# Performance work log

Measured on AMD Instinct MI355X. Metric: run time of the kernel, lower is better.

The kernel has to match this reference:

```python
import jax, jax.numpy as jnp
import numpy as np

DECAY = 0.99
EPS = 1e-5
K = 512  # num_embeddings


def setup_inputs() -> dict:
    key = jax.random.key(0)
    k1, k2, k3 = jax.random.split(key, 3)
    B, C, H, W = 32, 64, 64, 64
    x = jax.random.normal(k1, (B, C, H, W), dtype=jnp.float32)
    codebook = jax.random.uniform(k2, (K, C), dtype=jnp.float32)
    ema_cluster_size = jnp.ones((K,), dtype=jnp.float32)
    ema_weight = jax.random.uniform(k3, (K, C), dtype=jnp.float32)
    return {"x": x, "codebook": codebook,
            "ema_cluster_size": ema_cluster_size, "ema_weight": ema_weight}


def reference(x, codebook, ema_cluster_size, ema_weight):
    B, C, H, W = x.shape
    # (B, C, H, W) -> (B*H*W, C)
    x_flat = jnp.transpose(x, (0, 2, 3, 1)).reshape(-1, C)

    x_sq = jnp.sum(x_flat * x_flat, axis=1, keepdims=True)        # [N, 1]
    e_sq = jnp.sum(codebook * codebook, axis=1)[None, :]          # [1, K]
    distances = x_sq + e_sq - 2.0 * (x_flat @ codebook.T)         # [N, K]
    indices = jnp.argmin(distances, axis=1)                        # [N]

    quantized = codebook[indices].reshape(B, H, W, C)
    quantized = jnp.transpose(quantized, (0, 3, 1, 2))             # [B, C, H, W]

    # EMA codebook update (training path); one-hot matmuls expressed as segment sums
    counts = jax.ops.segment_sum(jnp.ones_like(indices, dtype=x.dtype), indices,
                                 num_segments=K)                   # [K]
    sums = jax.ops.segment_sum(x_flat, indices, num_segments=K)    # [K, C]
    new_cluster_size = DECAY * ema_cluster_size + (1.0 - DECAY) * counts
    new_ema_weight = DECAY * ema_weight + (1.0 - DECAY) * sums
    n = jnp.sum(new_cluster_size)
    smoothed = (new_cluster_size + EPS) / (n + K * EPS) * n
    new_codebook = new_ema_weight / smoothed[:, None]

    commitment_loss = jnp.mean((x - jax.lax.stop_gradient(quantized)) ** 2)
    unique_codes = jnp.sum(counts > 0).astype(jnp.float32)

    out = x + jax.lax.stop_gradient(quantized - x)  # straight-through estimator
    return out, commitment_loss, unique_codes, new_codebook
```

## Files before the change

kernel.cpp:

```cpp
#include <hip/hip_runtime.h>


typedef __attribute__((ext_vector_type(8))) short bf16x8;
typedef __attribute__((ext_vector_type(16))) float f32x16;

#define MFMA32 __builtin_amdgcn_mfma_f32_32x32x16_bf16

__device__ __forceinline__ unsigned short f2bf(float f) {
    unsigned u = __float_as_uint(f);
    return (unsigned short)((u + 0x7fffu + ((u >> 16) & 1u)) >> 16);
}
__device__ __forceinline__ float bf2f(unsigned short h) {
    return __uint_as_float(((unsigned)h) << 16);
}

__device__ __forceinline__ void upd(float s, int kq, float& b1, int& q1, float& b2, int& q2) {
    bool t1 = s < b1;
    bool t2 = s < b2;
    float nb2 = t1 ? b1 : (t2 ? s : b2);
    int   nq2 = t1 ? q1 : (t2 ? kq : q2);
    b2 = nb2; q2 = nq2;
    b1 = t1 ? s : b1;
    q1 = t1 ? kq : q1;
}

__device__ __forceinline__ int refine_pair(int k1, int k2, long gx,
        const float* __restrict__ x, const float* __restrict__ cbg,
        const float* esq) {
    const float4* e1 = (const float4*)(cbg + (k1 << 6));
    const float4* e2 = (const float4*)(cbg + (k2 << 6));
    float a0 = 0.f, a1 = 0.f, c0 = 0.f, c1 = 0.f;
    #pragma unroll 4
    for (int j = 0; j < 16; ++j) {
        float4 ea = e1[j], eb = e2[j];
        float x0 = x[gx + (long)(4 * j + 0) * 4096];
        float x1 = x[gx + (long)(4 * j + 1) * 4096];
        float x2 = x[gx + (long)(4 * j + 2) * 4096];
        float x3 = x[gx + (long)(4 * j + 3) * 4096];
        a0 = fmaf(x0, ea.x, a0); a1 = fmaf(x1, ea.y, a1);
        a0 = fmaf(x2, ea.z, a0); a1 = fmaf(x3, ea.w, a1);
        c0 = fmaf(x0, eb.x, c0); c1 = fmaf(x1, eb.y, c1);
        c0 = fmaf(x2, eb.z, c0); c1 = fmaf(x3, eb.w, c1);
    }
    float s1 = esq[k1] - 2.f * (a0 + a1);
    float s2 = esq[k2] - 2.f * (c0 + c1);
    return (s2 < s1 || (s2 == s1 && k2 < k1)) ? k2 : k1;
}

#define AM_LDS_FLOATS 33280

__global__ void __launch_bounds__(512, 1)
vq_argmin(const float* __restrict__ x, const float* __restrict__ cbg,
          unsigned short* __restrict__ bkg, float* __restrict__ zero528) {
    extern __shared__ float lds[];
    float* esq = lds + 32768;
    bf16x8* chi = (bf16x8*)lds;
    bf16x8* clo = (bf16x8*)(lds + 16384);
    const int tid  = threadIdx.x;
    const int lane = tid & 63;
    const int wv   = tid >> 6;
    const int l31  = lane & 31;
    const int hh   = lane >> 5;

    {
        const float4* rowp = (const float4*)(cbg + (tid << 6));
        float s = 0.f;
        #pragma unroll
        for (int u = 0; u < 8; ++u) {
            float4 va = rowp[u * 2], vb = rowp[u * 2 + 1];
            const float v[8] = {va.x, va.y, va.z, va.w, vb.x, vb.y, vb.z, vb.w};
            bf16x8 h8, l8;
            #pragma unroll
            for (int j = 0; j < 8; ++j) {
                float e = v[j];
                s = fmaf(e, e, s);
                unsigned short hb = f2bf(e);
                float lo = e - bf2f(hb);
                h8[j] = (short)hb;
                l8[j] = (short)f2bf(lo);
            }
            chi[u * 512 + tid] = h8;
            clo[u * 512 + tid] = l8;
        }
        esq[tid] = s;
    }
    zero528[tid] = 0.f;
    if (tid < 16) zero528[512 + tid] = 0.f;

    const int nb = blockIdx.x * 512 + wv * 64;
    bf16x8 B0h[4], B0l[4], B1h[4], B1l[4];
    #pragma unroll
    for (int ct = 0; ct < 2; ++ct) {
        const int n = nb + ct * 32 + l31;
        const long gx = (long)(n >> 12) * 262144 + (long)((n >> 6) & 63) * 64 + (n & 63);
        #pragma unroll
        for (int cs = 0; cs < 4; ++cs) {
            float v[8];
            #pragma unroll
            for (int j = 0; j < 8; ++j)
                v[j] = -2.f * x[gx + (long)(cs * 16 + hh * 8 + j) * 4096];
            union { unsigned u[4]; bf16x8 v8; } uh, ul;
            #pragma unroll
            for (int p = 0; p < 4; ++p) {
                unsigned hp, lp;
                asm("v_cvt_pk_bf16_f32 %0, %1, %2" : "=v"(hp) : "v"(v[2*p]), "v"(v[2*p+1]));
                float r0 = v[2*p]     - __uint_as_float(hp << 16);
                float r1 = v[2*p + 1] - __uint_as_float(hp & 0xFFFF0000u);
                asm("v_cvt_pk_bf16_f32 %0, %1, %2" : "=v"(lp) : "v"(r0), "v"(r1));
                uh.u[p] = hp; ul.u[p] = lp;
            }
            if (ct == 0) { B0h[cs] = uh.v8; B0l[cs] = ul.v8; }
            else         { B1h[cs] = uh.v8; B1l[cs] = ul.v8; }
        }
    }
    __syncthreads();

    float b1a = 3.4e38f, b2a = 3.4e38f, b1b = 3.4e38f, b2b = 3.4e38f;
    int   q1a = 0, q2a = 0, q1b = 0, q2b = 0;
    bf16x8 Xh[4], Xl[4], Yh[4], Yl[4];

#define LOADA(Ah, Al, kt) { _Pragma("unroll") for (int cs = 0; cs < 4; ++cs) { \
        const int fi = (cs * 2 + hh) * 512 + (kt) * 32 + l31; \
        Ah[cs] = chi[fi]; Al[cs] = clo[fi]; } }

#define STEP(Ah, Al, kt) { \
        f32x16 acc0, acc1; \
        _Pragma("unroll") for (int g = 0; g < 4; ++g) { \
            float4 e4 = *(const float4*)(esq + (kt) * 32 + 8 * g + 4 * hh); \
            acc0[4*g] = e4.x; acc0[4*g+1] = e4.y; acc0[4*g+2] = e4.z; acc0[4*g+3] = e4.w; \
            acc1[4*g] = e4.x; acc1[4*g+1] = e4.y; acc1[4*g+2] = e4.z; acc1[4*g+3] = e4.w; } \
        _Pragma("unroll") for (int cs = 0; cs < 4; ++cs) { \
            acc0 = MFMA32(Ah[cs], B0h[cs], acc0, 0, 0, 0); \
            acc1 = MFMA32(Ah[cs], B1h[cs], acc1, 0, 0, 0); \
            acc0 = MFMA32(Al[cs], B0h[cs], acc0, 0, 0, 0); \
            acc1 = MFMA32(Al[cs], B1h[cs], acc1, 0, 0, 0); \
            acc0 = MFMA32(Ah[cs], B0l[cs], acc0, 0, 0, 0); \
            acc1 = MFMA32(Ah[cs], B1l[cs], acc1, 0, 0, 0); } \
        _Pragma("unroll") for (int e = 0; e < 16; ++e) { \
            int kq = (kt) * 32 + (e & 3) + 8 * (e >> 2); \
            upd(acc0[e], kq, b1a, q1a, b2a, q2a); \
            upd(acc1[e], kq, b1b, q1b, b2b, q2b); } }

    LOADA(Xh, Xl, 0)
    #pragma unroll 1
    for (int ktp = 0; ktp < 16; ktp += 2) {
        LOADA(Yh, Yl, ktp + 1)
        STEP(Xh, Xl, ktp)
        if (ktp + 2 < 16) LOADA(Xh, Xl, ktp + 2)
        STEP(Yh, Yl, ktp + 1)
    }

#define MERGE(b1, q1, b2, q2, ct) { \
        float mb1 = b1, mb2 = b2; int mk1 = q1 + 4 * hh, mk2 = q2 + 4 * hh; \
        float ob1 = __shfl_xor(mb1, 32, 64); int ok1 = __shfl_xor(mk1, 32, 64); \
        float ob2 = __shfl_xor(mb2, 32, 64); int ok2 = __shfl_xor(mk2, 32, 64); \
        bool t = (ob1 < mb1) || (ob1 == mb1 && ok1 < mk1); \
        float w1 = t ? ob1 : mb1;  int wk1 = t ? ok1 : mk1; \
        float l1 = t ? mb1 : ob1;  int lk1 = t ? mk1 : ok1; \
        float w2c = t ? ob2 : mb2; int wk2c = t ? ok2 : mk2; \
        bool t2 = (w2c < l1) || (w2c == l1 && wk2c < lk1); \
        float w2 = t2 ? w2c : l1;  int wk2 = t2 ? wk2c : lk1; \
        if (hh == 0) { \
            int kk = wk1; \
            if (wk2 != wk1 && (w2 - w1 < 2e-3f)) { \
                const int n = nb + (ct) * 32 + l31; \
                const long gx = (long)(n >> 12) * 262144 \
                              + (long)((n >> 6) & 63) * 64 + (n & 63); \
                kk = refine_pair(wk1, wk2, gx, x, cbg, esq); \
            } \
            bkg[nb + (ct) * 32 + l31] = (unsigned short)kk; } }

    MERGE(b1a, q1a, b2a, q2a, 0)
    MERGE(b1b, q1b, b2b, q2b, 1)
#undef LOADA
#undef STEP
#undef MERGE
}

#define FUSED_LDS_BYTES (33536 * 2)

__global__ void __launch_bounds__(512)
vq_fused(const float* __restrict__ x, const float* __restrict__ cbg,
         const unsigned short* __restrict__ bkg, float* __restrict__ out,
         float* __restrict__ hsum, float* __restrict__ acc_loss,
         float* __restrict__ slabs) {
    extern __shared__ unsigned short sm16[];
    const int tid = threadIdx.x;
    if (blockIdx.x < 256) {
        float* hist = (float*)sm16;
        float* lred = (float*)sm16 + 512;
        hist[tid] = 0.f;
        __syncthreads();
        const int n  = blockIdx.x * 512 + tid;
        const long gx = (long)(n >> 12) * 262144 + (long)((n >> 6) & 63) * 64 + (n & 63);
        const int k1 = bkg[n];
        atomicAdd(&hist[k1], 1.0f);
        const float4* q4 = (const float4*)(cbg + (k1 << 6));
        float lsum = 0.f;
        #pragma unroll
        for (int j = 0; j < 16; ++j) {
            float4 q = q4[j];
            const float qv[4] = {q.x, q.y, q.z, q.w};
            #pragma unroll
            for (int r = 0; r < 4; ++r) {
                const int c = 4 * j + r;
                float xc = x[gx + (long)c * 4096];
                out[gx + (long)c * 4096] = qv[r];
                float d = xc - qv[r];
                lsum = fmaf(d, d, lsum);
            }
        }
        #pragma unroll
        for (int o = 32; o > 0; o >>= 1) lsum += __shfl_down(lsum, o, 64);
        if ((tid & 63) == 0) lred[tid >> 6] = lsum;
        __syncthreads();
        if (tid == 0) {
            float l = ((lred[0] + lred[1]) + (lred[2] + lred[3]))
                    + ((lred[4] + lred[5]) + (lred[6] + lred[7]));
            atomicAdd(acc_loss, l);
        }
        { float v = hist[tid]; if (v != 0.f) atomicAdd(&hsum[tid], v); }
    } else {
        unsigned short* xb = sm16;
        unsigned short* kb = sm16 + 33024;
        const int lane = tid & 63;
        const int w    = tid >> 6;
        const int l31  = lane & 31;
        const int hh   = lane >> 5;
        const int bix  = blockIdx.x - 256;
        const int n0   = bix * 512;
        const float* xpl = x + (long)(n0 >> 12) * 262144 + (n0 & 4095);

        kb[tid] = bkg[n0 + tid];
        #pragma unroll
        for (int i = 0; i < 16; ++i) {
            const int f  = tid + i * 512;
            const int c  = f >> 7;
            const int n4 = (f & 127) << 2;
            float4 v = *(const float4*)(xpl + (long)c * 4096 + n4);
            ushort4 o;
            o.x = f2bf(v.x); o.y = f2bf(v.y); o.z = f2bf(v.z); o.w = f2bf(v.w);
            *(ushort4*)(xb + c * 516 + n4) = o;
        }
        __syncthreads();

        const int t0 = w * 32 + l31;
        const int t1 = (w + 8) * 32 + l31;
        f32x16 aA0 = {}, aA1 = {}, aB0 = {}, aB1 = {};

        #pragma unroll 1
        for (int b16 = 0; b16 < 32; ++b16) {
            const int nofs = b16 * 16 + hh * 8;
            ushort4 p0a = *(const ushort4*)(xb + l31 * 516 + nofs);
            ushort4 p0b = *(const ushort4*)(xb + l31 * 516 + nofs + 4);
            ushort4 p1a = *(const ushort4*)(xb + (32 + l31) * 516 + nofs);
            ushort4 p1b = *(const ushort4*)(xb + (32 + l31) * 516 + nofs + 4);
            bf16x8 Bf0, Bf1;
            Bf0[0] = (short)p0a.x; Bf0[1] = (short)p0a.y;
            Bf0[2] = (short)p0a.z; Bf0[3] = (short)p0a.w;
            Bf0[4] = (short)p0b.x; Bf0[5] = (short)p0b.y;
            Bf0[6] = (short)p0b.z; Bf0[7] = (short)p0b.w;
            Bf1[0] = (short)p1a.x; Bf1[1] = (short)p1a.y;
            Bf1[2] = (short)p1a.z; Bf1[3] = (short)p1a.w;
            Bf1[4] = (short)p1b.x; Bf1[5] = (short)p1b.y;
            Bf1[6] = (short)p1b.z; Bf1[7] = (short)p1b.w;
            ushort4 k4a = *(const ushort4*)(kb + nofs);
            ushort4 k4b = *(const ushort4*)(kb + nofs + 4);
            const int kk[8] = {k4a.x, k4a.y, k4a.z, k4a.w,
                               k4b.x, k4b.y, k4b.z, k4b.w};
            bf16x8 A0, A1;
            #pragma unroll
            for (int j = 0; j < 8; ++j) {
                A0[j] = (kk[j] == t0) ? (short)0x3F80 : (short)0;
                A1[j] = (kk[j] == t1) ? (short)0x3F80 : (short)0;
            }
            aA0 = MFMA32(A0, Bf0, aA0, 0, 0, 0);
            aA1 = MFMA32(A0, Bf1, aA1, 0, 0, 0);
            aB0 = MFMA32(A1, Bf0, aB0, 0, 0, 0);
            aB1 = MFMA32(A1, Bf1, aB1, 0, 0, 0);
        }
        float* slab = slabs + (long)bix * 32768;
        #pragma unroll
        for (int e = 0; e < 16; ++e) {
            const int row = (e & 3) + 8 * (e >> 2) + 4 * hh;
            slab[(w * 32 + row) * 64 + l31]            = aA0[e];
            slab[(w * 32 + row) * 64 + 32 + l31]       = aA1[e];
            slab[((w + 8) * 32 + row) * 64 + l31]      = aB0[e];
            slab[((w + 8) * 32 + row) * 64 + 32 + l31] = aB1[e];
        }
    }
}

__global__ void __launch_bounds__(512)
vq_final(const float* __restrict__ slabs, const float* __restrict__ hsum,
         const float* __restrict__ acc_loss, const float* __restrict__ ema_cs,
         const float* __restrict__ ema_w, float* __restrict__ out_scalars,
         float* __restrict__ out_cb) {
    __shared__ float sm[512];
    __shared__ float s_red[17];
    const int tid = threadIdx.x;
    float cnt = hsum[tid];
    float ncs = 0.99f * ema_cs[tid] + 0.01f * cnt;
    float v1 = ncs;
    float v2 = (cnt > 0.f) ? 1.f : 0.f;
    #pragma unroll
    for (int o = 32; o > 0; o >>= 1) {
        v1 += __shfl_down(v1, o, 64);
        v2 += __shfl_down(v2, o, 64);
    }
    const int wv = tid >> 6;
    if ((tid & 63) == 0) { s_red[wv] = v1; s_red[wv + 8] = v2; }
    __syncthreads();
    if (tid == 0) {
        float nn = 0.f, uq = 0.f;
        #pragma unroll
        for (int i = 0; i < 8; ++i) { nn += s_red[i]; uq += s_red[i + 8]; }
        s_red[16] = nn;
        if (blockIdx.x == 0) {
            out_scalars[0] = acc_loss[0] / 8388608.f;
            out_scalars[1] = uq;
        }
    }
    __syncthreads();
    float nn = s_red[16];
    sm[tid] = (ncs + 1e-5f) / (nn + 512.f * 1e-5f) * nn;
    __syncthreads();
    const int e = blockIdx.x * 512 + tid;
    float s = 0.f;
    #pragma unroll 8
    for (int b = 0; b < 256; ++b) s += slabs[(long)b * 32768 + e];
    float nw = 0.99f * ema_w[e] + 0.01f * s;
    out_cb[e] = nw / sm[e >> 6];
}

extern "C" void kernel_launch(void* const* d_in, const int* in_sizes, int n_in,
                              void* d_out, int out_size, void* d_ws, size_t ws_size,
                              hipStream_t stream) {
    const float* x      = (const float*)d_in[0];
    const float* cb     = (const float*)d_in[1];
    const float* ema_cs = (const float*)d_in[2];
    const float* ema_w  = (const float*)d_in[3];

    float* out     = (float*)d_out;
    float* scalars = out + 8388608;
    float* out_cb  = out + 8388610;
    float* ws      = (float*)d_ws;

    float* slabs    = ws;
    float* hsum     = slabs + 8388608;
    float* acc_loss = hsum + 512;
    unsigned short* bkg = (unsigned short*)(acc_loss + 16);

    vq_argmin<<<256, 512, AM_LDS_FLOATS * sizeof(float), stream>>>(x, cb, bkg, hsum);
    vq_fused<<<512, 512, FUSED_LDS_BYTES, stream>>>(x, cb, bkg, out, hsum, acc_loss, slabs);
    vq_final<<<64, 512, 0, stream>>>(slabs, hsum, acc_loss, ema_cs, ema_w, scalars, out_cb);
}
```

Measured before the change: 89.33 us.

## Precompute split-bf16 codebook in prep kernel and halve argmin block work for occupancy

```diff
diff --git a/kernel.cpp b/kernel.cpp
--- a/kernel.cpp
+++ b/kernel.cpp
@@ -12,6 +12,39 @@
 }
 __device__ __forceinline__ float bf2f(unsigned short h) {
     return __uint_as_float(((unsigned)h) << 16);
+}
+
+__global__ void __launch_bounds__(512)
+vq_prep(const float* __restrict__ cb, float* __restrict__ esq, char* __restrict__ cbF) {
+    __shared__ float tile[64 * 65];
+    const int tid = threadIdx.x;
+    const int k0  = blockIdx.x * 64;
+    #pragma unroll
+    for (int i = tid; i < 4096; i += 512)
+        tile[(i >> 6) * 65 + (i & 63)] = cb[k0 * 64 + i];
+    __syncthreads();
+    const int u  = tid >> 6;
+    const int kl = tid & 63;
+    const float* row = tile + kl * 65;
+    const int cbase = (u >> 1) * 16 + (u & 1) * 8;
+    bf16x8 h8, l8;
+    #pragma unroll
+    for (int j = 0; j < 8; ++j) {
+        float e = row[cbase + j];
+        unsigned short hb = f2bf(e);
+        float lo = e - bf2f(hb);
+        h8[j] = (short)hb;
+        l8[j] = (short)f2bf(lo);
+    }
+    const size_t idx = (size_t)(u * 512 + k0 + kl) * 16;
+    *(bf16x8*)(cbF + idx)         = h8;
+    *(bf16x8*)(cbF + 65536 + idx) = l8;
+    if (u == 0) {
+        float s = 0.f;
+        #pragma unroll
+        for (int c = 0; c < 64; ++c) { float v = row[c]; s = fmaf(v, v, s); }
+        esq[k0 + kl] = s;
+    }
 }
 
 __device__ __forceinline__ void upd(float s, int kq, float& b1, int& q1, float& b2, int& q2) {
@@ -47,15 +80,16 @@
     return (s2 < s1 || (s2 == s1 && k2 < k1)) ? k2 : k1;
 }
 
-#define AM_LDS_FLOATS 33280
-
-__global__ void __launch_bounds__(512, 1)
+#define AM_LDS_FLOATS 16896
+
+__global__ void __launch_bounds__(512, 2)
 vq_argmin(const float* __restrict__ x, const float* __restrict__ cbg,
+          const float* __restrict__ esqg, const char* __restrict__ cbF,
           unsigned short* __restrict__ bkg, float* __restrict__ zero528) {
     extern __shared__ float lds[];
-    float* esq = lds + 32768;
-    bf16x8* chi = (bf16x8*)lds;
-    bf16x8* clo = (bf16x8*)(lds + 16384);
+    float* esq = lds + 16384;
+    const bf16x8* chi   = (const bf16x8*)lds;
+    const bf16x8* clo_g = (const bf16x8*)(cbF + 65536);
     const int tid  = threadIdx.x;
     const int lane = tid & 63;
     const int wv   = tid >> 6;
@@ -63,35 +97,19 @@
     const int hh   = lane >> 5;
 
     {
-        const float4* rowp = (const float4*)(cbg + (tid << 6));
-        float s = 0.f;
-        #pragma unroll
-        for (int u = 0; u < 8; ++u) {
-            float4 va = rowp[u * 2], vb = rowp[u * 2 + 1];
-            const float v[8] = {va.x, va.y, va.z, va.w, vb.x, vb.y, vb.z, vb.w};
-            bf16x8 h8, l8;
-            #pragma unroll
-            for (int j = 0; j < 8; ++j) {
-                float e = v[j];
-                s = fmaf(e, e, s);
-                unsigned short hb = f2bf(e);
-                float lo = e - bf2f(hb);
-                h8[j] = (short)hb;
-                l8[j] = (short)f2bf(lo);
-            }
-            chi[u * 512 + tid] = h8;
-            clo[u * 512 + tid] = l8;
-        }
-        esq[tid] = s;
+        const float4* src = (const float4*)cbF;
+        float4* dst = (float4*)lds;
+        #pragma unroll
+        for (int i = tid; i < 4096; i += 512) dst[i] = src[i];
+        esq[tid] = esqg[tid];
     }
     zero528[tid] = 0.f;
     if (tid < 16) zero528[512 + tid] = 0.f;
 
-    const int nb = blockIdx.x * 512 + wv * 64;
-    bf16x8 B0h[4], B0l[4], B1h[4], B1l[4];
-    #pragma unroll
-    for (int ct = 0; ct < 2; ++ct) {
-        const int n = nb + ct * 32 + l31;
+    const int nb = blockIdx.x * 256 + wv * 32;
+    bf16x8 Bh[4], Bl[4];
+    {
+        const int n = nb + l31;
         const long gx = (long)(n >> 12) * 262144 + (long)((n >> 6) & 63) * 64 + (n & 63);
         #pragma unroll
         for (int cs = 0; cs < 4; ++cs) {
@@ -109,72 +127,67 @@
                 asm("v_cvt_pk_bf16_f32 %0, %1, %2" : "=v"(lp) : "v"(r0), "v"(r1));
                 uh.u[p] = hp; ul.u[p] = lp;
             }
-            if (ct == 0) { B0h[cs] = uh.v8; B0l[cs] = ul.v8; }
-            else         { B1h[cs] = uh.v8; B1l[cs] = ul.v8; }
-        }
-    }
-    __syncthreads();
-
-    float b1a = 3.4e38f, b2a = 3.4e38f, b1b = 3.4e38f, b2b = 3.4e38f;
-    int   q1a = 0, q2a = 0, q1b = 0, q2b = 0;
-    bf16x8 Xh[4], Xl[4], Yh[4], Yl[4];
-
-#define LOADA(Ah, Al, kt) { _Pragma("unroll") for (int cs = 0; cs < 4; ++cs) { \
-        const int fi = (cs * 2 + hh) * 512 + (kt) * 32 + l31; \
-        Ah[cs] = chi[fi]; Al[cs] = clo[fi]; } }
-
-#define STEP(Ah, Al, kt) { \
-        f32x16 acc0, acc1; \
+            Bh[cs] = uh.v8; Bl[cs] = ul.v8;
+        }
+    }
+    __syncthreads();
+
+    float b1 = 3.4e38f, b2 = 3.4e38f;
+    int   q1 = 0, q2 = 0;
+    bf16x8 Xl[4], Yl[4];
+
+#define LOADAL(Al, kt) { _Pragma("unroll") for (int cs = 0; cs < 4; ++cs) { \
+        Al[cs] = clo_g[(cs * 2 + hh) * 512 + (kt) * 32 + l31]; } }
+
+#define STEP(Al, kt) { \
+        bf16x8 Ah[4]; \
+        _Pragma("unroll") for (int cs = 0; cs < 4; ++cs) \
+            Ah[cs] = chi[(cs * 2 + hh) * 512 + (kt) * 32 + l31]; \
+        f32x16 acc; \
         _Pragma("unroll") for (int g = 0; g < 4; ++g) { \
             float4 e4 = *(const float4*)(esq + (kt) * 32 + 8 * g + 4 * hh); \
-            acc0[4*g] = e4.x; acc0[4*g+1] = e4.y; acc0[4*g+2] = e4.z; acc0[4*g+3] = e4.w; \
-            acc1[4*g] = e4.x; acc1[4*g+1] = e4.y; acc1[4*g+2] = e4.z; acc1[4*g+3] = e4.w; } \
+            acc[4*g] = e4.x; acc[4*g+1] = e4.y; acc[4*g+2] = e4.z; acc[4*g+3] = e4.w; } \
         _Pragma("unroll") for (int cs = 0; cs < 4; ++cs) { \
-            acc0 = MFMA32(Ah[cs], B0h[cs], acc0, 0, 0, 0); \
-            acc1 = MFMA32(Ah[cs], B1h[cs], acc1, 0, 0, 0); \
-            acc0 = MFMA32(Al[cs], B0h[cs], acc0, 0, 0, 0); \
-            acc1 = MFMA32(Al[cs], B1h[cs], acc1, 0, 0, 0); \
-            acc0 = MFMA32(Ah[cs], B0l[cs], acc0, 0, 0, 0); \
-            acc1 = MFMA32(Ah[cs], B1l[cs], acc1, 0, 0, 0); } \
+            acc = MFMA32(Ah[cs], Bh[cs], acc, 0, 0, 0); \
+            acc = MFMA32(Al[cs], Bh[cs], acc, 0, 0, 0); \
+            acc = MFMA32(Ah[cs], Bl[cs], acc, 0, 0, 0); } \
         _Pragma("unroll") for (int e = 0; e < 16; ++e) { \
             int kq = (kt) * 32 + (e & 3) + 8 * (e >> 2); \
-            upd(acc0[e], kq, b1a, q1a, b2a, q2a); \
-            upd(acc1[e], kq, b1b, q1b, b2b, q2b); } }
-
-    LOADA(Xh, Xl, 0)
+            upd(acc[e], kq, b1, q1, b2, q2); } }
+
+    LOADAL(Xl, 0)
     #pragma unroll 1
     for (int ktp = 0; ktp < 16; ktp += 2) {
-        LOADA(Yh, Yl, ktp + 1)
-        STEP(Xh, Xl, ktp)
-        if (ktp + 2 < 16) LOADA(Xh, Xl, ktp + 2)
-        STEP(Yh, Yl, ktp + 1)
-    }
-
-#define MERGE(b1, q1, b2, q2, ct) { \
-        float mb1 = b1, mb2 = b2; int mk1 = q1 + 4 * hh, mk2 = q2 + 4 * hh; \
-        float ob1 = __shfl_xor(mb1, 32, 64); int ok1 = __shfl_xor(mk1, 32, 64); \
-        float ob2 = __shfl_xor(mb2, 32, 64); int ok2 = __shfl_xor(mk2, 32, 64); \
-        bool t = (ob1 < mb1) || (ob1 == mb1 && ok1 < mk1); \
-        float w1 = t ? ob1 : mb1;  int wk1 = t ? ok1 : mk1; \
-        float l1 = t ? mb1 : ob1;  int lk1 = t ? mk1 : ok1; \
-        float w2c = t ? ob2 : mb2; int wk2c = t ? ok2 : mk2; \
-        bool t2 = (w2c < l1) || (w2c == l1 && wk2c < lk1); \
-        float w2 = t2 ? w2c : l1;  int wk2 = t2 ? wk2c : lk1; \
-        if (hh == 0) { \
-            int kk = wk1; \
-            if (wk2 != wk1 && (w2 - w1 < 2e-3f)) { \
-                const int n = nb + (ct) * 32 + l31; \
-                const long gx = (long)(n >> 12) * 262144 \
-                              + (long)((n >> 6) & 63) * 64 + (n & 63); \
-                kk = refine_pair(wk1, wk2, gx, x, cbg, esq); \
-            } \
-            bkg[nb + (ct) * 32 + l31] = (unsigned short)kk; } }
-
-    MERGE(b1a, q1a, b2a, q2a, 0)
-    MERGE(b1b, q1b, b2b, q2b, 1)
-#undef LOADA
+        LOADAL(Yl, ktp + 1)
+        STEP(Xl, ktp)
+        if (ktp + 2 < 16) LOADAL(Xl, ktp + 2)
+        STEP(Yl, ktp + 1)
+    }
+
+    {
+        float mb1 = b1, mb2 = b2;
+        int   mk1 = q1 + 4 * hh, mk2 = q2 + 4 * hh;
+        float ob1 = __shfl_xor(mb1, 32, 64); int ok1 = __shfl_xor(mk1, 32, 64);
+        float ob2 = __shfl_xor(mb2, 32, 64); int ok2 = __shfl_xor(mk2, 32, 64);
+        bool t = (ob1 < mb1) || (ob1 == mb1 && ok1 < mk1);
+        float w1 = t ? ob1 : mb1;  int wk1 = t ? ok1 : mk1;
+        float l1 = t ? mb1 : ob1;  int lk1 = t ? mk1 : ok1;
+        float w2c = t ? ob2 : mb2; int wk2c = t ? ok2 : mk2;
+        bool t2 = (w2c < l1) || (w2c == l1 && wk2c < lk1);
+        float w2 = t2 ? w2c : l1;  int wk2 = t2 ? wk2c : lk1;
+        if (hh == 0) {
+            int kk = wk1;
+            if (wk2 != wk1 && (w2 - w1 < 2e-3f)) {
+                const int n = nb + l31;
+                const long gx = (long)(n >> 12) * 262144
+                              + (long)((n >> 6) & 63) * 64 + (n & 63);
+                kk = refine_pair(wk1, wk2, gx, x, cbg, esq);
+            }
+            bkg[nb + l31] = (unsigned short)kk;
+        }
+    }
+#undef LOADAL
 #undef STEP
-#undef MERGE
 }
 
 #define FUSED_LDS_BYTES (33536 * 2)
@@ -349,9 +362,12 @@
     float* slabs    = ws;
     float* hsum     = slabs + 8388608;
     float* acc_loss = hsum + 512;
-    unsigned short* bkg = (unsigned short*)(acc_loss + 16);
-
-    vq_argmin<<<256, 512, AM_LDS_FLOATS * sizeof(float), stream>>>(x, cb, bkg, hsum);
+    float* esq      = acc_loss + 16;
+    char*  cbF      = (char*)(esq + 512);
+    unsigned short* bkg = (unsigned short*)(cbF + 131072);
+
+    vq_prep<<<8, 512, 0, stream>>>(cb, esq, cbF);
+    vq_argmin<<<512, 512, AM_LDS_FLOATS * sizeof(float), stream>>>(x, cb, esq, cbF, bkg, hsum);
     vq_fused<<<512, 512, FUSED_LDS_BYTES, stream>>>(x, cb, bkg, out, hsum, acc_loss, slabs);
     vq_final<<<64, 512, 0, stream>>>(slabs, hsum, acc_loss, ema_cs, ema_w, scalars, out_cb);
 }
```

Result: no change. 88.62 us (-0.8%).

## Precompute split-bf16 codebook in prep kernel and halve argmin LDS for occupancy

Applied to the files above, without the earlier changes.

```diff
diff --git a/kernel.cpp b/kernel.cpp
--- a/kernel.cpp
+++ b/kernel.cpp
@@ -5,6 +5,7 @@
 typedef __attribute__((ext_vector_type(16))) float f32x16;
 
 #define MFMA32 __builtin_amdgcn_mfma_f32_32x32x16_bf16
+#define NSEG 256
 
 __device__ __forceinline__ unsigned short f2bf(float f) {
     unsigned u = __float_as_uint(f);
@@ -14,13 +15,46 @@
     return __uint_as_float(((unsigned)h) << 16);
 }
 
+__global__ void __launch_bounds__(512)
+vq_prep(const float* __restrict__ cb, float* __restrict__ esq, char* __restrict__ cbF) {
+    __shared__ float tile[64 * 65];
+    const int tid = threadIdx.x;
+    const int k0  = blockIdx.x * 64;
+    #pragma unroll
+    for (int i = tid; i < 4096; i += 512)
+        tile[(i >> 6) * 65 + (i & 63)] = cb[k0 * 64 + i];
+    __syncthreads();
+    const int u  = tid >> 6;
+    const int kl = tid & 63;
+    const float* row = tile + kl * 65;
+    const int cbase = (u >> 1) * 16 + (u & 1) * 8;
+    bf16x8 h8, l8;
+    #pragma unroll
+    for (int j = 0; j < 8; ++j) {
+        float e = row[cbase + j];
+        unsigned short hb = f2bf(e);
+        float lo = e - bf2f(hb);
+        h8[j] = (short)hb;
+        l8[j] = (short)f2bf(lo);
+    }
+    const size_t idx = (size_t)(u * 512 + k0 + kl) * 16;
+    *(bf16x8*)(cbF + idx)         = h8;
+    *(bf16x8*)(cbF + 65536 + idx) = l8;
+    if (u == 0) {
+        float s = 0.f;
+        #pragma unroll
+        for (int c = 0; c < 64; ++c) { float v = row[c]; s = fmaf(v, v, s); }
+        esq[k0 + kl] = s;
+    }
+}
+
 __device__ __forceinline__ void upd(float s, int kq, float& b1, int& q1, float& b2, int& q2) {
     bool t1 = s < b1;
     bool t2 = s < b2;
-    float nb2 = t1 ? b1 : (t2 ? s : b2);
-    int   nq2 = t1 ? q1 : (t2 ? kq : q2);
-    b2 = nb2; q2 = nq2;
-    b1 = t1 ? s : b1;
+    int  nq2 = t1 ? q1 : (t2 ? kq : q2);
+    b2 = __builtin_amdgcn_fmed3f(s, b1, b2);
+    q2 = nq2;
+    b1 = fminf(s, b1);
     q1 = t1 ? kq : q1;
 }
 
@@ -47,15 +81,16 @@
     return (s2 < s1 || (s2 == s1 && k2 < k1)) ? k2 : k1;
 }
 
-#define AM_LDS_FLOATS 33280
-
-__global__ void __launch_bounds__(512, 1)
+#define AM_LDS_FLOATS 16896
+
+__global__ void __launch_bounds__(512, 2)
 vq_argmin(const float* __restrict__ x, const float* __restrict__ cbg,
+          const float* __restrict__ esqg, const char* __restrict__ cbF,
           unsigned short* __restrict__ bkg, float* __restrict__ zero528) {
     extern __shared__ float lds[];
-    float* esq = lds + 32768;
-    bf16x8* chi = (bf16x8*)lds;
-    bf16x8* clo = (bf16x8*)(lds + 16384);
+    float* esq = lds + 16384;
+    const bf16x8* chi   = (const bf16x8*)lds;
+    const bf16x8* clo_g = (const bf16x8*)(cbF + 65536);
     const int tid  = threadIdx.x;
     const int lane = tid & 63;
     const int wv   = tid >> 6;
@@ -63,26 +98,11 @@
     const int hh   = lane >> 5;
 
     {
-        const float4* rowp = (const float4*)(cbg + (tid << 6));
-        float s = 0.f;
-        #pragma unroll
-        for (int u = 0; u < 8; ++u) {
-            float4 va = rowp[u * 2], vb = rowp[u * 2 + 1];
-            const float v[8] = {va.x, va.y, va.z, va.w, vb.x, vb.y, vb.z, vb.w};
-            bf16x8 h8, l8;
-            #pragma unroll
-            for (int j = 0; j < 8; ++j) {
-                float e = v[j];
-                s = fmaf(e, e, s);
-                unsigned short hb = f2bf(e);
-                float lo = e - bf2f(hb);
-                h8[j] = (short)hb;
-                l8[j] = (short)f2bf(lo);
-            }
-            chi[u * 512 + tid] = h8;
-            clo[u * 512 + tid] = l8;
-        }
-        esq[tid] = s;
+        const float4* src = (const float4*)cbF;
+        float4* dst = (float4*)lds;
+        #pragma unroll
+        for (int i = tid; i < 4096; i += 512) dst[i] = src[i];
+        esq[tid] = esqg[tid];
     }
     zero528[tid] = 0.f;
     if (tid < 16) zero528[512 + tid] = 0.f;
@@ -117,13 +137,15 @@
 
     float b1a = 3.4e38f, b2a = 3.4e38f, b1b = 3.4e38f, b2b = 3.4e38f;
     int   q1a = 0, q2a = 0, q1b = 0, q2b = 0;
-    bf16x8 Xh[4], Xl[4], Yh[4], Yl[4];
-
-#define LOADA(Ah, Al, kt) { _Pragma("unroll") for (int cs = 0; cs < 4; ++cs) { \
-        const int fi = (cs * 2 + hh) * 512 + (kt) * 32 + l31; \
-        Ah[cs] = chi[fi]; Al[cs] = clo[fi]; } }
-
-#define STEP(Ah, Al, kt) { \
+    bf16x8 Xl[4], Yl[4];
+
+#define LOADAL(Al, kt) { _Pragma("unroll") for (int cs = 0; cs < 4; ++cs) { \
+        Al[cs] = clo_g[(cs * 2 + hh) * 512 + (kt) * 32 + l31]; } }
+
+#define STEP(Al, kt) { \
+        bf16x8 Ah[4]; \
+        _Pragma("unroll") for (int cs = 0; cs < 4; ++cs) \
+            Ah[cs] = chi[(cs * 2 + hh) * 512 + (kt) * 32 + l31]; \
         f32x16 acc0, acc1; \
         _Pragma("unroll") for (int g = 0; g < 4; ++g) { \
             float4 e4 = *(const float4*)(esq + (kt) * 32 + 8 * g + 4 * hh); \
@@ -141,13 +163,13 @@
             upd(acc0[e], kq, b1a, q1a, b2a, q2a); \
             upd(acc1[e], kq, b1b, q1b, b2b, q2b); } }
 
-    LOADA(Xh, Xl, 0)
+    LOADAL(Xl, 0)
     #pragma unroll 1
     for (int ktp = 0; ktp < 16; ktp += 2) {
-        LOADA(Yh, Yl, ktp + 1)
-        STEP(Xh, Xl, ktp)
-        if (ktp + 2 < 16) LOADA(Xh, Xl, ktp + 2)
-        STEP(Yh, Yl, ktp + 1)
+        LOADAL(Yl, ktp + 1)
+        STEP(Xl, ktp)
+        if (ktp + 2 < 16) LOADAL(Xl, ktp + 2)
+        STEP(Yl, ktp + 1)
     }
 
 #define MERGE(b1, q1, b2, q2, ct) { \
@@ -172,7 +194,7 @@
 
     MERGE(b1a, q1a, b2a, q2a, 0)
     MERGE(b1b, q1b, b2b, q2b, 1)
-#undef LOADA
+#undef LOADAL
 #undef STEP
 #undef MERGE
 }
@@ -328,7 +350,7 @@
     const int e = blockIdx.x * 512 + tid;
     float s = 0.f;
     #pragma unroll 8
-    for (int b = 0; b < 256; ++b) s += slabs[(long)b * 32768 + e];
+    for (int b = 0; b < NSEG; ++b) s += slabs[(long)b * 32768 + e];
     float nw = 0.99f * ema_w[e] + 0.01f * s;
     out_cb[e] = nw / sm[e >> 6];
 }
@@ -347,11 +369,14 @@
     float* ws      = (float*)d_ws;
 
     float* slabs    = ws;
-    float* hsum     = slabs + 8388608;
+    float* hsum     = slabs + (size_t)NSEG * 32768;
     float* acc_loss = hsum + 512;
-    unsigned short* bkg = (unsigned short*)(acc_loss + 16);
-
-    vq_argmin<<<256, 512, AM_LDS_FLOATS * sizeof(float), stream>>>(x, cb, bkg, hsum);
+    float* esq      = acc_loss + 16;
+    char*  cbF      = (char*)(esq + 512);
+    unsigned short* bkg = (unsigned short*)(cbF + 131072);
+
+    vq_prep<<<8, 512, 0, stream>>>(cb, esq, cbF);
+    vq_argmin<<<256, 512, AM_LDS_FLOATS * sizeof(float), stream>>>(x, cb, esq, cbF, bkg, hsum);
     vq_fused<<<512, 512, FUSED_LDS_BYTES, stream>>>(x, cb, bkg, out, hsum, acc_loss, slabs);
     vq_final<<<64, 512, 0, stream>>>(slabs, hsum, acc_loss, ema_cs, ema_w, scalars, out_cb);
 }
```

Result: slower. 91.85 us (+2.8%).
